# Performance work log

Hardware: AMD Instinct MI355X
Metric: run time of the kernel (lower is better)

## Reference

```python
import jax, jax.numpy as jnp
import numpy as np

N = 200000      # total nodes
H = 256         # hidden dim
G = 512         # number of graphs (segments)


def setup_inputs() -> dict:
    key = jax.random.key(0)
    ks = jax.random.split(key, 6)
    x = jax.random.normal(ks[0], (N, H), dtype=jnp.float32)
    batch = jnp.sort(jax.random.randint(ks[1], (N,), 0, G, dtype=jnp.int64))
    # attn_gate: Linear(H, H//2) -> Tanh -> Linear(H//2, 1)
    W1 = jax.random.normal(ks[2], (H, H // 2), dtype=jnp.float32) * (1.0 / np.sqrt(H))
    b1 = jnp.zeros((H // 2,), dtype=jnp.float32)
    W2 = jax.random.normal(ks[3], (H // 2, 1), dtype=jnp.float32) * (1.0 / np.sqrt(H // 2))
    b2 = jnp.zeros((1,), dtype=jnp.float32)
    # context_proj: Linear(H, H)
    Wp = jax.random.normal(ks[4], (H, H), dtype=jnp.float32) * (1.0 / np.sqrt(H))
    bp = jnp.zeros((H,), dtype=jnp.float32)
    return {"x": x, "batch": batch, "W1": W1, "b1": b1, "W2": W2, "b2": b2, "Wp": Wp, "bp": bp}


def reference(x, batch, W1, b1, W2, b2, Wp, bp):
    # gating MLP -> per-node scalar score [N, 1]
    s = jnp.tanh(x @ W1 + b1) @ W2 + b2
    # scatter_softmax over segments (numerically stable)
    seg_max = jax.ops.segment_max(s, batch, num_segments=G)        # [G, 1]
    e = jnp.exp(s - seg_max[batch])                                 # [N, 1]
    seg_sum = jax.ops.segment_sum(e, batch, num_segments=G)        # [G, 1]
    w = e / seg_sum[batch]                                          # [N, 1]
    # attention-weighted global add pool -> [G, H]
    graph_emb = jax.ops.segment_sum(x * w, batch, num_segments=G)
    # project and broadcast back to nodes -> [N, H]
    context = graph_emb @ Wp + bp
    return context[batch]
```

## Files before the change

kernel.cpp:

```cpp
#include <hip/hip_runtime.h>
#include <hip/hip_bf16.h>

#define HH 256
#define HJ 128
#define GG 512

typedef __attribute__((ext_vector_type(8))) short short8;
typedef __attribute__((ext_vector_type(4))) float f32x4;

static __device__ __forceinline__ unsigned f2bfu(float f) {
  unsigned u = __builtin_bit_cast(unsigned, f);
  return (u + 0x7FFFu + ((u >> 16) & 1u)) >> 16;
}

static __device__ __forceinline__ uint2 pack4(const float4 f) {
  return make_uint2(f2bfu(f.x) | (f2bfu(f.y) << 16),
                    f2bfu(f.z) | (f2bfu(f.w) << 16));
}

static __device__ __forceinline__ float fast_tanh_pos2e(float e2h) {
  return 1.f - 2.f * __builtin_amdgcn_rcpf(e2h + 1.f);
}

__global__ __launch_bounds__(64) void w1frag_kernel(
    const float* __restrict__ W1, short8* __restrict__ w1a) {
  const int l = threadIdx.x;
  const int kt = blockIdx.x >> 3;
  const int jt = blockIdx.x & 7;
  const int j = jt * 16 + (l & 15);
  const int kb = kt * 32 + (l >> 4) * 8;
  short8 v;
#pragma unroll
  for (int i = 0; i < 8; ++i) v[i] = (short)f2bfu(W1[(size_t)(kb + i) * HJ + j]);
  w1a[blockIdx.x * 64 + l] = v;
}

__global__ __launch_bounds__(256) void segstart_kernel(
    const int* __restrict__ batch, int* __restrict__ segstart, int N, int G) {
  const int n = blockIdx.x * 256 + threadIdx.x;
  if (n >= N) return;
  const int b = batch[n];
  const int p = (n == 0) ? -1 : batch[n - 1];
  for (int g = p + 1; g <= b; ++g) segstart[g] = n;
  if (n == N - 1) {
    for (int g = b + 1; g <= G; ++g) segstart[g] = N;
  }
}

__global__ __launch_bounds__(512) void fused_kernel(
    const float* __restrict__ x, const short8* __restrict__ w1a,
    const float* __restrict__ b1, const float* __restrict__ W2,
    const int* __restrict__ segstart, const float* __restrict__ Wp,
    const float* __restrict__ bp, f32x4* __restrict__ out4, int N) {
  __shared__ char xb[3 * 32768];
  __shared__ float spart[2][8][64];
  __shared__ float elds[64];
  __shared__ float esums;

  const int tid = threadIdx.x;
  const int l = tid & 63;
  const int w = tid >> 6;
  const int g = blockIdx.x;

  const int n0 = segstart[g];
  const int n1 = segstart[g + 1];
  const int cnt = n1 - n0;
  if (cnt <= 0) return;

  const int ntiles = (cnt + 63) >> 6;
  const float4* x4 = (const float4*)x;

  const int jt0 = w & 3;
  short8 afrag[2][8];
  float4 bb[2], ww[2];
  if (w < 4) {
#pragma unroll
    for (int jj = 0; jj < 2; ++jj) {
      const int jt = jt0 + jj * 4;
#pragma unroll
      for (int kt = 0; kt < 8; ++kt) afrag[jj][kt] = w1a[(kt * 8 + jt) * 64 + l];
      const int j0 = 16 * jt + (l >> 4) * 4;
      bb[jj] = *reinterpret_cast<const float4*>(b1 + j0);
      ww[jj] = *reinterpret_cast<const float4*>(W2 + j0);
    }
  }

  {
    float4 rr[8];
#pragma unroll
    for (int k = 0; k < 8; ++k) {
      const int node = min(n0 + w * 8 + k, N - 1);
      rr[k] = x4[(size_t)node * 64 + l];
    }
#pragma unroll
    for (int k = 0; k < 8; ++k) {
      const int r = w * 8 + k;
      const int swz = (r & 7) << 4;
      *reinterpret_cast<uint2*>(xb + r * 512 + ((l * 8) ^ swz)) = pack4(rr[k]);
    }
  }
  __syncthreads();

  const int c2 = tid & 127;
  const int qh = (tid >> 7) & 1;
  float2 pacc = make_float2(0.f, 0.f);
  float es_acc = 0.f;

  for (int i = 0; i < ntiles; ++i) {
    if (w < 4) {
      const char* xbi = xb + (i % 3) * 32768;
      float* sp = &spart[i & 1][0][0];
#pragma unroll
      for (int nt = 0; nt < 4; ++nt) {
        const int node = nt * 16 + (l & 15);
        const int nb = node * 512;
        const int swz = (node & 7) << 4;
        short8 bfrag[8];
#pragma unroll
        for (int kt = 0; kt < 8; ++kt) {
          bfrag[kt] = *reinterpret_cast<const short8*>(
              xbi + nb + ((kt * 64 + ((l >> 4) << 4)) ^ swz));
        }
#pragma unroll
        for (int jj = 0; jj < 2; ++jj) {
          f32x4 acc = (f32x4)(0.f);
#pragma unroll
          for (int kt = 0; kt < 8; ++kt) {
            acc = __builtin_amdgcn_mfma_f32_16x16x32_bf16(afrag[jj][kt],
                                                          bfrag[kt], acc, 0, 0, 0);
          }
          float t0 = __expf(2.f * (acc[0] + bb[jj].x));
          float t1 = __expf(2.f * (acc[1] + bb[jj].y));
          float t2 = __expf(2.f * (acc[2] + bb[jj].z));
          float t3 = __expf(2.f * (acc[3] + bb[jj].w));
          float ps = fast_tanh_pos2e(t0) * ww[jj].x +
                     fast_tanh_pos2e(t1) * ww[jj].y +
                     fast_tanh_pos2e(t2) * ww[jj].z +
                     fast_tanh_pos2e(t3) * ww[jj].w;
          ps += __shfl_xor(ps, 16, 64);
          ps += __shfl_xor(ps, 32, 64);
          if (l < 16) sp[(jt0 + jj * 4) * 64 + node] = ps;
        }
      }
    } else {
      if (i >= 1) {
        const float* sp = &spart[(i - 1) & 1][0][0];
        float s = 0.f;
#pragma unroll
        for (int jt = 0; jt < 8; ++jt) s += sp[jt * 64 + l];
        const int node = n0 + (i - 1) * 64 + l;
        const float e = (node < n1) ? __expf(s) : 0.f;
        elds[l] = e;
        if (w == 4) es_acc += e;
        const char* xbs = xb + ((i - 1) % 3) * 32768;
#pragma unroll 8
        for (int m = 0; m < 32; ++m) {
          const int n = qh * 32 + m;
          const unsigned v = *reinterpret_cast<const unsigned*>(
              xbs + n * 512 + ((c2 * 4) ^ ((n & 7) << 4)));
          const float ee = elds[n];
          pacc.x = fmaf(__builtin_bit_cast(float, v << 16), ee, pacc.x);
          pacc.y = fmaf(__builtin_bit_cast(float, v & 0xFFFF0000u), ee, pacc.y);
        }
      }
      if (i + 1 < ntiles) {
        char* xbd = xb + ((i + 1) % 3) * 32768;
        const int rb = (w - 4) * 16;
        float4 rr[8];
#pragma unroll
        for (int b = 0; b < 2; ++b) {
#pragma unroll
          for (int k = 0; k < 8; ++k) {
            const int node = min(n0 + (i + 1) * 64 + rb + b * 8 + k, N - 1);
            rr[k] = x4[(size_t)node * 64 + l];
          }
#pragma unroll
          for (int k = 0; k < 8; ++k) {
            const int r = rb + b * 8 + k;
            const int swz = (r & 7) << 4;
            *reinterpret_cast<uint2*>(xbd + r * 512 + ((l * 8) ^ swz)) =
                pack4(rr[k]);
          }
        }
      }
    }
    __syncthreads();
  }

  if (w >= 4) {
    const float* sp = &spart[(ntiles - 1) & 1][0][0];
    float s = 0.f;
#pragma unroll
    for (int jt = 0; jt < 8; ++jt) s += sp[jt * 64 + l];
    const int node = n0 + (ntiles - 1) * 64 + l;
    const float e = (node < n1) ? __expf(s) : 0.f;
    elds[l] = e;
    if (w == 4) es_acc += e;
    const char* xbs = xb + ((ntiles - 1) % 3) * 32768;
#pragma unroll 8
    for (int m = 0; m < 32; ++m) {
      const int n = qh * 32 + m;
      const unsigned v = *reinterpret_cast<const unsigned*>(
          xbs + n * 512 + ((c2 * 4) ^ ((n & 7) << 4)));
      const float ee = elds[n];
      pacc.x = fmaf(__builtin_bit_cast(float, v << 16), ee, pacc.x);
      pacc.y = fmaf(__builtin_bit_cast(float, v & 0xFFFF0000u), ee, pacc.y);
    }
    if (w == 4) {
      float es = es_acc;
      es += __shfl_xor(es, 1, 64);
      es += __shfl_xor(es, 2, 64);
      es += __shfl_xor(es, 4, 64);
      es += __shfl_xor(es, 8, 64);
      es += __shfl_xor(es, 16, 64);
      es += __shfl_xor(es, 32, 64);
      if (l == 0) esums = es;
    }
  }
  __syncthreads();

  float* fbase = (float*)xb;
  if (w >= 4) {
    fbase[qh * 256 + c2 * 2] = pacc.x;
    fbase[qh * 256 + c2 * 2 + 1] = pacc.y;
  }
  __syncthreads();

  float* er = fbase + 512;
  if (tid < HH) {
    const float es = esums;
    const float inv = (es > 0.f) ? 1.f / es : 0.f;
    er[tid] = (fbase[tid] + fbase[256 + tid]) * inv;
  }
  __syncthreads();

  float* pr = fbase + 768;
  {
    const int c = tid & 255;
    const int h2 = tid >> 8;
    float p = 0.f;
    const float* wp = Wp + (size_t)h2 * 128 * HH + c;
#pragma unroll 4
    for (int k = 0; k < 128; ++k) {
      p = fmaf(er[h2 * 128 + k], wp[(size_t)k * HH], p);
    }
    pr[h2 * 256 + c] = p;
  }
  __syncthreads();
  float* ctxl = fbase + 1280;
  if (tid < HH) {
    ctxl[tid] = pr[tid] + pr[256 + tid] + bp[tid];
  }
  __syncthreads();

  {
    const int q = tid & 63;
    const f32x4 cv = reinterpret_cast<const f32x4*>(ctxl)[q];
    for (int n = n0 + w; n < n1; n += 8) {
      __builtin_nontemporal_store(cv, &out4[(size_t)n * 64 + q]);
    }
  }
}

extern "C" void kernel_launch(void* const* d_in, const int* in_sizes, int n_in,
                              void* d_out, int out_size, void* d_ws, size_t ws_size,
                              hipStream_t stream) {
  const float* x = (const float*)d_in[0];
  const int* batch = (const int*)d_in[1];
  const float* W1 = (const float*)d_in[2];
  const float* b1 = (const float*)d_in[3];
  const float* W2 = (const float*)d_in[4];
  const float* Wp = (const float*)d_in[6];
  const float* bp = (const float*)d_in[7];
  float* out = (float*)d_out;

  const int N = in_sizes[1];
  const int G = GG;

  char* wsp = (char*)d_ws;
  short8* w1a = (short8*)wsp;
  size_t off = 4096 * sizeof(short8);
  int* segstart = (int*)(wsp + off);

  w1frag_kernel<<<dim3(64), 64, 0, stream>>>(W1, w1a);
  {
    dim3 grid((N + 255) / 256);
    segstart_kernel<<<grid, 256, 0, stream>>>(batch, segstart, N, G);
  }
  fused_kernel<<<dim3(G), 512, 0, stream>>>(x, w1a, b1, W2, segstart, Wp, bp,
                                            (f32x4*)out, N);
}
```

Measured before the change: 104.8 us.

## Process two graphs per block and overlap output broadcast with next graph's pass

Each block now handles two consecutive segments. The broadcast stores of the previous graph's context vector are interleaved into the loader warps' work during the next graph's tile loop, with any leftover rows written afterward. This aims to hide the large output write behind the x reads and the MFMA work. In exchange the grid is halved to 256 blocks, which cuts parallelism on a GPU with many CUs and serialises the two graphs inside each block.

```diff
diff --git a/kernel.cpp b/kernel.cpp
--- a/kernel.cpp
+++ b/kernel.cpp
@@ -56,18 +56,11 @@
   __shared__ float spart[2][8][64];
   __shared__ float elds[64];
   __shared__ float esums;
+  __shared__ float ctxp[HH];
 
   const int tid = threadIdx.x;
   const int l = tid & 63;
   const int w = tid >> 6;
-  const int g = blockIdx.x;
-
-  const int n0 = segstart[g];
-  const int n1 = segstart[g + 1];
-  const int cnt = n1 - n0;
-  if (cnt <= 0) return;
-
-  const int ntiles = (cnt + 63) >> 6;
   const float4* x4 = (const float4*)x;
 
   const int jt0 = w & 3;
@@ -85,179 +78,212 @@
     }
   }
 
-  {
-    float4 rr[8];
-#pragma unroll
-    for (int k = 0; k < 8; ++k) {
-      const int node = min(n0 + w * 8 + k, N - 1);
-      rr[k] = x4[(size_t)node * 64 + l];
-    }
-#pragma unroll
-    for (int k = 0; k < 8; ++k) {
-      const int r = w * 8 + k;
-      const int swz = (r & 7) << 4;
-      *reinterpret_cast<uint2*>(xb + r * 512 + ((l * 8) ^ swz)) = pack4(rr[k]);
-    }
-  }
-  __syncthreads();
-
   const int c2 = tid & 127;
   const int qh = (tid >> 7) & 1;
-  float2 pacc = make_float2(0.f, 0.f);
-  float es_acc = 0.f;
-
-  for (int i = 0; i < ntiles; ++i) {
-    if (w < 4) {
-      const char* xbi = xb + (i % 3) * 32768;
-      float* sp = &spart[i & 1][0][0];
-#pragma unroll
-      for (int nt = 0; nt < 4; ++nt) {
-        const int node = nt * 16 + (l & 15);
-        const int nb = node * 512;
-        const int swz = (node & 7) << 4;
-        short8 bfrag[8];
-#pragma unroll
-        for (int kt = 0; kt < 8; ++kt) {
-          bfrag[kt] = *reinterpret_cast<const short8*>(
-              xbi + nb + ((kt * 64 + ((l >> 4) << 4)) ^ swz));
+
+  int pn0 = 0, pn1 = 0;
+  bool pvalid = false;
+
+  for (int gi = 0; gi < 2; ++gi) {
+    const int g = blockIdx.x * 2 + gi;
+    const int n0 = segstart[g];
+    const int n1 = segstart[g + 1];
+    const int cnt = n1 - n0;
+    if (cnt <= 0) continue;
+
+    const int ntiles = (cnt + 63) >> 6;
+
+    {
+      float4 rr[8];
+#pragma unroll
+      for (int k = 0; k < 8; ++k) {
+        const int node = min(n0 + w * 8 + k, N - 1);
+        rr[k] = x4[(size_t)node * 64 + l];
+      }
+#pragma unroll
+      for (int k = 0; k < 8; ++k) {
+        const int r = w * 8 + k;
+        const int swz = (r & 7) << 4;
+        *reinterpret_cast<uint2*>(xb + r * 512 + ((l * 8) ^ swz)) = pack4(rr[k]);
+      }
+    }
+    __syncthreads();
+
+    f32x4 cvp;
+    if (pvalid) cvp = reinterpret_cast<const f32x4*>(ctxp)[l];
+
+    float2 pacc = make_float2(0.f, 0.f);
+    float es_acc = 0.f;
+
+    for (int i = 0; i < ntiles; ++i) {
+      if (w < 4) {
+        const char* xbi = xb + (i % 3) * 32768;
+        float* sp = &spart[i & 1][0][0];
+#pragma unroll
+        for (int nt = 0; nt < 4; ++nt) {
+          const int node = nt * 16 + (l & 15);
+          const int nb = node * 512;
+          const int swz = (node & 7) << 4;
+          short8 bfrag[8];
+#pragma unroll
+          for (int kt = 0; kt < 8; ++kt) {
+            bfrag[kt] = *reinterpret_cast<const short8*>(
+                xbi + nb + ((kt * 64 + ((l >> 4) << 4)) ^ swz));
+          }
+#pragma unroll
+          for (int jj = 0; jj < 2; ++jj) {
+            f32x4 acc = (f32x4)(0.f);
+#pragma unroll
+            for (int kt = 0; kt < 8; ++kt) {
+              acc = __builtin_amdgcn_mfma_f32_16x16x32_bf16(afrag[jj][kt],
+                                                            bfrag[kt], acc, 0, 0, 0);
+            }
+            float t0 = __expf(2.f * (acc[0] + bb[jj].x));
+            float t1 = __expf(2.f * (acc[1] + bb[jj].y));
+            float t2 = __expf(2.f * (acc[2] + bb[jj].z));
+            float t3 = __expf(2.f * (acc[3] + bb[jj].w));
+            float ps = fast_tanh_pos2e(t0) * ww[jj].x +
+                       fast_tanh_pos2e(t1) * ww[jj].y +
+                       fast_tanh_pos2e(t2) * ww[jj].z +
+                       fast_tanh_pos2e(t3) * ww[jj].w;
+            ps += __shfl_xor(ps, 16, 64);
+            ps += __shfl_xor(ps, 32, 64);
+            if (l < 16) sp[(jt0 + jj * 4) * 64 + node] = ps;
+          }
         }
-#pragma unroll
-        for (int jj = 0; jj < 2; ++jj) {
-          f32x4 acc = (f32x4)(0.f);
-#pragma unroll
-          for (int kt = 0; kt < 8; ++kt) {
-            acc = __builtin_amdgcn_mfma_f32_16x16x32_bf16(afrag[jj][kt],
-                                                          bfrag[kt], acc, 0, 0, 0);
-          }
-          float t0 = __expf(2.f * (acc[0] + bb[jj].x));
-          float t1 = __expf(2.f * (acc[1] + bb[jj].y));
-          float t2 = __expf(2.f * (acc[2] + bb[jj].z));
-          float t3 = __expf(2.f * (acc[3] + bb[jj].w));
-          float ps = fast_tanh_pos2e(t0) * ww[jj].x +
-                     fast_tanh_pos2e(t1) * ww[jj].y +
-                     fast_tanh_pos2e(t2) * ww[jj].z +
-                     fast_tanh_pos2e(t3) * ww[jj].w;
-          ps += __shfl_xor(ps, 16, 64);
-          ps += __shfl_xor(ps, 32, 64);
-          if (l < 16) sp[(jt0 + jj * 4) * 64 + node] = ps;
+      } else {
+        if (i >= 1) {
+          const float* sp = &spart[(i - 1) & 1][0][0];
+          float s = 0.f;
+#pragma unroll
+          for (int jt = 0; jt < 8; ++jt) s += sp[jt * 64 + l];
+          const int node = n0 + (i - 1) * 64 + l;
+          const float e = (node < n1) ? __expf(s) : 0.f;
+          elds[l] = e;
+          if (w == 4) es_acc += e;
+          const char* xbs = xb + ((i - 1) % 3) * 32768;
+#pragma unroll 8
+          for (int m = 0; m < 32; ++m) {
+            const int n = qh * 32 + m;
+            const unsigned v = *reinterpret_cast<const unsigned*>(
+                xbs + n * 512 + ((c2 * 4) ^ ((n & 7) << 4)));
+            const float ee = elds[n];
+            pacc.x = fmaf(__builtin_bit_cast(float, v << 16), ee, pacc.x);
+            pacc.y = fmaf(__builtin_bit_cast(float, v & 0xFFFF0000u), ee, pacc.y);
+          }
         }
-      }
-    } else {
-      if (i >= 1) {
-        const float* sp = &spart[(i - 1) & 1][0][0];
-        float s = 0.f;
-#pragma unroll
-        for (int jt = 0; jt < 8; ++jt) s += sp[jt * 64 + l];
-        const int node = n0 + (i - 1) * 64 + l;
-        const float e = (node < n1) ? __expf(s) : 0.f;
-        elds[l] = e;
-        if (w == 4) es_acc += e;
-        const char* xbs = xb + ((i - 1) % 3) * 32768;
+        if (i + 1 < ntiles) {
+          char* xbd = xb + ((i + 1) % 3) * 32768;
+          const int rb = (w - 4) * 16;
+          float4 rr[8];
+#pragma unroll
+          for (int b = 0; b < 2; ++b) {
+#pragma unroll
+            for (int k = 0; k < 8; ++k) {
+              const int node = min(n0 + (i + 1) * 64 + rb + b * 8 + k, N - 1);
+              rr[k] = x4[(size_t)node * 64 + l];
+            }
+#pragma unroll
+            for (int k = 0; k < 8; ++k) {
+              const int r = rb + b * 8 + k;
+              const int swz = (r & 7) << 4;
+              *reinterpret_cast<uint2*>(xbd + r * 512 + ((l * 8) ^ swz)) =
+                  pack4(rr[k]);
+            }
+          }
+        }
+        if (pvalid) {
+          const int rbase = i * 64 + (w - 4) * 16;
+#pragma unroll 4
+          for (int k = 0; k < 16; ++k) {
+            const int n = pn0 + rbase + k;
+            if (n < pn1) {
+              __builtin_nontemporal_store(cvp, &out4[(size_t)n * 64 + l]);
+            }
+          }
+        }
+      }
+      __syncthreads();
+    }
+
+    if (w >= 4) {
+      const float* sp = &spart[(ntiles - 1) & 1][0][0];
+      float s = 0.f;
+#pragma unroll
+      for (int jt = 0; jt < 8; ++jt) s += sp[jt * 64 + l];
+      const int node = n0 + (ntiles - 1) * 64 + l;
+      const float e = (node < n1) ? __expf(s) : 0.f;
+      elds[l] = e;
+      if (w == 4) es_acc += e;
+      const char* xbs = xb + ((ntiles - 1) % 3) * 32768;
 #pragma unroll 8
-        for (int m = 0; m < 32; ++m) {
-          const int n = qh * 32 + m;
-          const unsigned v = *reinterpret_cast<const unsigned*>(
-              xbs + n * 512 + ((c2 * 4) ^ ((n & 7) << 4)));
-          const float ee = elds[n];
-          pacc.x = fmaf(__builtin_bit_cast(float, v << 16), ee, pacc.x);
-          pacc.y = fmaf(__builtin_bit_cast(float, v & 0xFFFF0000u), ee, pacc.y);
-        }
-      }
-      if (i + 1 < ntiles) {
-        char* xbd = xb + ((i + 1) % 3) * 32768;
-        const int rb = (w - 4) * 16;
-        float4 rr[8];
-#pragma unroll
-        for (int b = 0; b < 2; ++b) {
-#pragma unroll
-          for (int k = 0; k < 8; ++k) {
-            const int node = min(n0 + (i + 1) * 64 + rb + b * 8 + k, N - 1);
-            rr[k] = x4[(size_t)node * 64 + l];
-          }
-#pragma unroll
-          for (int k = 0; k < 8; ++k) {
-            const int r = rb + b * 8 + k;
-            const int swz = (r & 7) << 4;
-            *reinterpret_cast<uint2*>(xbd + r * 512 + ((l * 8) ^ swz)) =
-                pack4(rr[k]);
-          }
-        }
-      }
-    }
-    __syncthreads();
-  }
-
-  if (w >= 4) {
-    const float* sp = &spart[(ntiles - 1) & 1][0][0];
-    float s = 0.f;
-#pragma unroll
-    for (int jt = 0; jt < 8; ++jt) s += sp[jt * 64 + l];
-    const int node = n0 + (ntiles - 1) * 64 + l;
-    const float e = (node < n1) ? __expf(s) : 0.f;
-    elds[l] = e;
-    if (w == 4) es_acc += e;
-    const char* xbs = xb + ((ntiles - 1) % 3) * 32768;
-#pragma unroll 8
-    for (int m = 0; m < 32; ++m) {
-      const int n = qh * 32 + m;
-      const unsigned v = *reinterpret_cast<const unsigned*>(
-          xbs + n * 512 + ((c2 * 4) ^ ((n & 7) << 4)));
-      const float ee = elds[n];
-      pacc.x = fmaf(__builtin_bit_cast(float, v << 16), ee, pacc.x);
-      pacc.y = fmaf(__builtin_bit_cast(float, v & 0xFFFF0000u), ee, pacc.y);
-    }
-    if (w == 4) {
-      float es = es_acc;
-      es += __shfl_xor(es, 1, 64);
-      es += __shfl_xor(es, 2, 64);
-      es += __shfl_xor(es, 4, 64);
-      es += __shfl_xor(es, 8, 64);
-      es += __shfl_xor(es, 16, 64);
-      es += __shfl_xor(es, 32, 64);
-      if (l == 0) esums = es;
-    }
-  }
-  __syncthreads();
-
-  float* fbase = (float*)xb;
-  if (w >= 4) {
-    fbase[qh * 256 + c2 * 2] = pacc.x;
-    fbase[qh * 256 + c2 * 2 + 1] = pacc.y;
-  }
-  __syncthreads();
-
-  float* er = fbase + 512;
-  if (tid < HH) {
-    const float es = esums;
-    const float inv = (es > 0.f) ? 1.f / es : 0.f;
-    er[tid] = (fbase[tid] + fbase[256 + tid]) * inv;
-  }
-  __syncthreads();
-
-  float* pr = fbase + 768;
-  {
-    const int c = tid & 255;
-    const int h2 = tid >> 8;
-    float p = 0.f;
-    const float* wp = Wp + (size_t)h2 * 128 * HH + c;
+      for (int m = 0; m < 32; ++m) {
+        const int n = qh * 32 + m;
+        const unsigned v = *reinterpret_cast<const unsigned*>(
+            xbs + n * 512 + ((c2 * 4) ^ ((n & 7) << 4)));
+        const float ee = elds[n];
+        pacc.x = fmaf(__builtin_bit_cast(float, v << 16), ee, pacc.x);
+        pacc.y = fmaf(__builtin_bit_cast(float, v & 0xFFFF0000u), ee, pacc.y);
+      }
+      if (w == 4) {
+        float es = es_acc;
+        es += __shfl_xor(es, 1, 64);
+        es += __shfl_xor(es, 2, 64);
+        es += __shfl_xor(es, 4, 64);
+        es += __shfl_xor(es, 8, 64);
+        es += __shfl_xor(es, 16, 64);
+        es += __shfl_xor(es, 32, 64);
+        if (l == 0) esums = es;
+      }
+    } else if (pvalid) {
+      const f32x4 cvl = reinterpret_cast<const f32x4*>(ctxp)[l];
+      for (int n = pn0 + ntiles * 64 + w; n < pn1; n += 4) {
+        __builtin_nontemporal_store(cvl, &out4[(size_t)n * 64 + l]);
+      }
+    }
+    __syncthreads();
+
+    float* fbase = (float*)xb;
+    if (w >= 4) {
+      fbase[qh * 256 + c2 * 2] = pacc.x;
+      fbase[qh * 256 + c2 * 2 + 1] = pacc.y;
+    }
+    __syncthreads();
+
+    float* er = fbase + 512;
+    if (tid < HH) {
+      const float es = esums;
+      const float inv = (es > 0.f) ? 1.f / es : 0.f;
+      er[tid] = (fbase[tid] + fbase[256 + tid]) * inv;
+    }
+    __syncthreads();
+
+    float* pr = fbase + 768;
+    {
+      const int c = tid & 255;
+      const int h2 = tid >> 8;
+      float p = 0.f;
+      const float* wp = Wp + (size_t)h2 * 128 * HH + c;
 #pragma unroll 4
-    for (int k = 0; k < 128; ++k) {
-      p = fmaf(er[h2 * 128 + k], wp[(size_t)k * HH], p);
-    }
-    pr[h2 * 256 + c] = p;
-  }
-  __syncthreads();
-  float* ctxl = fbase + 1280;
-  if (tid < HH) {
-    ctxl[tid] = pr[tid] + pr[256 + tid] + bp[tid];
-  }
-  __syncthreads();
-
-  {
-    const int q = tid & 63;
-    const f32x4 cv = reinterpret_cast<const f32x4*>(ctxl)[q];
-    for (int n = n0 + w; n < n1; n += 8) {
-      __builtin_nontemporal_store(cv, &out4[(size_t)n * 64 + q]);
+      for (int k = 0; k < 128; ++k) {
+        p = fmaf(er[h2 * 128 + k], wp[(size_t)k * HH], p);
+      }
+      pr[h2 * 256 + c] = p;
+    }
+    __syncthreads();
+    if (tid < HH) {
+      ctxp[tid] = pr[tid] + pr[256 + tid] + bp[tid];
+    }
+    pn0 = n0;
+    pn1 = n1;
+    pvalid = true;
+    __syncthreads();
+  }
+
+  if (pvalid) {
+    const f32x4 cv = reinterpret_cast<const f32x4*>(ctxp)[l];
+    for (int n = pn0 + w; n < pn1; n += 8) {
+      __builtin_nontemporal_store(cv, &out4[(size_t)n * 64 + l]);
     }
   }
 }
@@ -287,6 +313,6 @@
     dim3 grid((N + 255) / 256);
     segstart_kernel<<<grid, 256, 0, stream>>>(batch, segstart, N, G);
   }
-  fused_kernel<<<dim3(G), 512, 0, stream>>>(x, w1a, b1, W2, segstart, Wp, bp,
-                                            (f32x4*)out, N);
-}
+  fused_kernel<<<dim3(G / 2), 512, 0, stream>>>(x, w1a, b1, W2, segstart, Wp,
+                                                bp, (f32x4*)out, N);
+}
```

Result: faster. 94.48 us (median of 2 runs) (-9.9%).
